# Optimization experiments

Measured on AMD Instinct MI355X. Metric: run time of the kernel, lower is better.

## Reference

```python
import jax, jax.numpy as jnp
import numpy as np

N_HEADS = 8  # head_dim = 640 / 8 = 80


def _split_heads(x):
    # [B, S, D] -> [B, H, S, D/H]
    B, S, D = x.shape
    return x.reshape(B, S, N_HEADS, D // N_HEADS).transpose(0, 2, 1, 3)


def _merge_heads(x):
    # [B, H, S, d] -> [B, S, H*d]
    B, H, S, d = x.shape
    return x.transpose(0, 2, 1, 3).reshape(B, S, H * d)


def setup_inputs() -> dict:
    key = jax.random.key(0)
    ks = jax.random.split(key, 12)
    B, S, D, C, A = 4, 2048, 640, 768, 16

    def w(k, fan_in, fan_out, s=1.0):
        return (jax.random.normal(k, (fan_in, fan_out), jnp.float32) / np.sqrt(fan_in) * s)

    return {
        "hidden_states": jax.random.normal(ks[0], (B, S, D), jnp.float32),
        "au_embedding": jax.random.normal(ks[1], (B, A, C), jnp.float32),
        "w_q": w(ks[2], D, D),
        "w_k": w(ks[3], D, D),
        "w_v": w(ks[4], D, D),
        "w_ak": w(ks[5], C, D),
        "w_av": w(ks[6], C, D),
        "w_g1": w(ks[7], D, D // 2),
        "b_g1": jnp.zeros((D // 2,), jnp.float32),
        "w_g2": w(ks[8], D // 2, D, s=0.02),  # near-zero per nn.init.zeros_
        "b_g2": jnp.full((D,), -1.5, jnp.float32),  # per nn.init.constant_(-1.5)
        "w_out": w(ks[9], D, D),
        "b_out": jnp.zeros((D,), jnp.float32),
        "temperature": jnp.full((1,), 5.0, jnp.float32),
    }


def reference(hidden_states, au_embedding, w_q, w_k, w_v, w_ak, w_av,
              w_g1, b_g1, w_g2, b_g2, w_out, b_out, temperature):
    au_scale = 1.0
    residual = hidden_states

    q = _split_heads(hidden_states @ w_q)  # [B,H,S,d]
    k = _split_heads(hidden_states @ w_k)
    v = _split_heads(hidden_states @ w_v)
    d = q.shape[-1]
    scale = 1.0 / jnp.sqrt(jnp.asarray(d, q.dtype))  # attn.scale = head_dim**-0.5

    # main self-attention: QK^T * scale -> softmax -> PV
    probs = jax.nn.softmax(jnp.einsum('bhqd,bhkd->bhqk', q, k) * scale, axis=-1)
    hs = _merge_heads(jnp.einsum('bhqk,bhkd->bhqd', probs, v))  # [B,S,D]

    # AU cross-attention with temperature-scaled logits
    au_k = _split_heads(au_embedding @ w_ak)  # [B,H,A,d]
    au_v = _split_heads(au_embedding @ w_av)
    scaled_alpha = scale * temperature[0]
    au_probs = jax.nn.softmax(jnp.einsum('bhqd,bhkd->bhqk', q, au_k) * scaled_alpha, axis=-1)
    au_hs = _merge_heads(jnp.einsum('bhqk,bhkd->bhqd', au_probs, au_v))  # [B,S,D]

    # gated MLP fusion: sigmoid(Linear(SiLU(Linear(au_hs))))
    gate = jax.nn.sigmoid(jax.nn.silu(au_hs @ w_g1 + b_g1) @ w_g2 + b_g2)
    hs = hs + au_scale * (gate * au_hs)

    hs = hs @ w_out + b_out  # to_out[0]; to_out[1] dropout is identity in eval
    return hs + residual  # residual_connection=True, rescale_output_factor=1.0
```

## Files before the change

### kernel.cpp

```cpp
#include <hip/hip_runtime.h>
#include <stdint.h>

typedef __attribute__((ext_vector_type(8))) short short8;
typedef __attribute__((ext_vector_type(4))) short short4v;
typedef __attribute__((ext_vector_type(4))) float f32x4;
typedef __attribute__((ext_vector_type(2))) uint32_t u32x2;

#define DEV static __device__ __forceinline__

DEV short f2bf(float f) {
  union { float f; uint32_t u; } v; v.f = f;
  uint32_t r = (v.u + 0x7fffu + ((v.u >> 16) & 1u)) >> 16;
  return (short)(uint16_t)r;
}
DEV float bf2f(short s) {
  union { uint32_t u; float f; } v; v.u = ((uint32_t)(uint16_t)s) << 16;
  return v.f;
}
DEV uint32_t fbits(float f) { union { float f; uint32_t u; } v; v.f = f; return v.u; }
DEV int imin(int a, int b) { return a < b ? a : b; }
DEV int xcd_swz(int bid, int nwg) {
  int q8 = nwg >> 3, r8 = nwg & 7;
  int xcd = bid & 7, lin = bid >> 3;
  return (xcd < r8 ? xcd * (q8 + 1) : r8 * (q8 + 1) + (xcd - r8) * q8) + lin;
}
DEV int detect_flag(const uint32_t* src, int t) {
  __shared__ int cnt;
  if (t == 0) cnt = 0;
  __syncthreads();
  uint32_t u = src[t & 255];
  int e = (int)((u >> 7) & 0xffu);
  if (e >= 110 && e <= 135) atomicAdd(&cnt, 1);
  __syncthreads();
  return cnt > 128;
}


struct WDesc { const void* src; short* dst; int K, N, dstride, tile0; };
struct WTable { WDesc d[8]; };

__global__ __launch_bounds__(256) void k_prep(
    const void* __restrict__ hidden, const void* __restrict__ auemb,
    short* __restrict__ HSB, short* __restrict__ AUB, WTable tb,
    const void* b1, const void* b2, const void* b3, const void* tp,
    float* B1, float* B2, float* B3, float* T) {
  const int t = threadIdx.x;
  const int isbf = detect_flag((const uint32_t*)hidden, t);
  const int bid = blockIdx.x;

  if (bid < 5168) {
    int i = bid * 256 + t;
    const void* src; short* dst;
    if (i < 1310720) { src = hidden; dst = HSB; }
    else { src = auemb; dst = AUB; i -= 1310720; }
    if (isbf) {
      ((short4v*)dst)[i] = ((const short4v*)src)[i];
    } else {
      f32x4 v = ((const f32x4*)src)[i];
      short4v o;
      o[0] = f2bf(v[0]); o[1] = f2bf(v[1]); o[2] = f2bf(v[2]); o[3] = f2bf(v[3]);
      ((short4v*)dst)[i] = o;
    }
  } else if (bid < 8128) {
    __shared__ float tile[32][33];
    int tid = bid - 5168;
    int idx = 0;
#pragma unroll
    for (int i = 1; i < 8; i++) if (tid >= tb.d[i].tile0) idx = i;
    WDesc wd = tb.d[idx];
    int local = tid - wd.tile0;
    int ntiles = wd.N >> 5;
    int n0 = (local % ntiles) * 32, k0 = (local / ntiles) * 32;
    int tx = t & 31, ty = t >> 5;
#pragma unroll
    for (int i = 0; i < 4; i++) {
      int r = k0 + ty + i * 8, c = n0 + tx;
      float v = 0.f;
      if (r < wd.K && c < wd.N)
        v = isbf ? bf2f(((const short*)wd.src)[(size_t)r * wd.N + c])
                 : ((const float*)wd.src)[(size_t)r * wd.N + c];
      tile[ty + i * 8][tx] = v;
    }
    __syncthreads();
#pragma unroll
    for (int i = 0; i < 4; i++) {
      int n = n0 + ty + i * 8, k = k0 + tx;
      if (n < wd.N && k < wd.K) wd.dst[(size_t)n * wd.dstride + k] = f2bf(tile[tx][ty + i * 8]);
    }
  } else {
    int i = (bid - 8128) * 256 + t;
    const void* s; float* d; int j;
    if (i < 320) { s = b1; d = B1; j = i; }
    else if (i < 960) { s = b2; d = B2; j = i - 320; }
    else if (i < 1600) { s = b3; d = B3; j = i - 960; }
    else if (i == 1600) { s = tp; d = T; j = 0; }
    else return;
    d[j] = isbf ? bf2f(((const short*)s)[j]) : ((const float*)s)[j];
  }
}

template <int EPI>
DEV void gemm_core(const short* __restrict__ A, const short* __restrict__ Wt,
                   void* __restrict__ Cout, int M, int N, int K, int m0, int n0,
                   const float* __restrict__ bias, const short* __restrict__ x1,
                   const short* __restrict__ x2, const short* __restrict__ res) {
  __shared__ __align__(16) short As[128 * 64];
  __shared__ __align__(16) short Bs[128 * 64];
  const int t = threadIdx.x;
  const int w = t >> 6, ln = t & 63;
  const int wm = w >> 1, wn = w & 1;
  const int lrow = ln & 15, lg = ln >> 4;

  f32x4 acc[4][4];
#pragma unroll
  for (int i = 0; i < 4; i++)
#pragma unroll
    for (int j = 0; j < 4; j++) acc[i][j] = (f32x4){0.f, 0.f, 0.f, 0.f};

  for (int k0 = 0; k0 < K; k0 += 64) {
    __syncthreads();
#pragma unroll
    for (int c = 0; c < 4; c++) {
      int cc = c * 256 + t;
      int r = cc >> 3, col = (cc & 7) * 8;
      int ra = imin(m0 + r, M - 1);
      int rb = imin(n0 + r, N - 1);
      __builtin_amdgcn_global_load_lds(
          (const __attribute__((address_space(1))) void*)(A + (size_t)ra * K + k0 + col),
          (__attribute__((address_space(3))) void*)&As[(c * 256 + w * 64) * 8],
          16, 0, 0);
      __builtin_amdgcn_global_load_lds(
          (const __attribute__((address_space(1))) void*)(Wt + (size_t)rb * K + k0 + col),
          (__attribute__((address_space(3))) void*)&Bs[(c * 256 + w * 64) * 8],
          16, 0, 0);
    }
    __syncthreads();
    short8 af[4][2], bfr[4][2];
#pragma unroll
    for (int i = 0; i < 4; i++)
#pragma unroll
      for (int kk = 0; kk < 2; kk++) {
        af[i][kk] = *(const short8*)&As[(wm * 64 + i * 16 + lrow) * 64 + lg * 8 + kk * 32];
        bfr[i][kk] = *(const short8*)&Bs[(wn * 64 + i * 16 + lrow) * 64 + lg * 8 + kk * 32];
      }
    __builtin_amdgcn_s_setprio(1);
#pragma unroll
    for (int kk = 0; kk < 2; kk++)
#pragma unroll
      for (int i = 0; i < 4; i++)
#pragma unroll
        for (int j = 0; j < 4; j++)
          acc[i][j] = __builtin_amdgcn_mfma_f32_16x16x32_bf16(af[i][kk], bfr[j][kk], acc[i][j], 0, 0, 0);
    __builtin_amdgcn_s_setprio(0);
  }

  const int rb0 = m0 + wm * 64 + lg * 4;
#pragma unroll
  for (int i = 0; i < 4; i++) {
#pragma unroll
    for (int j = 0; j < 4; j++) {
      int col = n0 + wn * 64 + j * 16 + lrow;
      if (col >= N) continue;
#pragma unroll
      for (int r = 0; r < 4; r++) {
        int row = rb0 + i * 16 + r;
        if (row >= M) continue;
        float v = acc[i][j][r];
        size_t off = (size_t)row * N + col;
        if (EPI == 0) {
          ((short*)Cout)[off] = f2bf(v);
        } else if (EPI == 1) {
          float x = v + bias[col];
          ((short*)Cout)[off] = f2bf(x / (1.f + __expf(-x)));
        } else if (EPI == 2) {
          float g = 1.f / (1.f + __expf(-(v + bias[col])));
          ((short*)Cout)[off] = f2bf(bf2f(x1[off]) + g * bf2f(x2[off]));
        } else {
          ((float*)Cout)[off] = v + bias[col] + bf2f(res[off]);
        }
      }
    }
  }
}

template <int EPI>
__global__ __launch_bounds__(256) void k_gemm_bt(
    const short* __restrict__ A, const short* __restrict__ Wt, void* __restrict__ Cout,
    int M, int N, int K, int nbx,
    const float* __restrict__ bias, const short* __restrict__ x1,
    const short* __restrict__ x2, const short* __restrict__ res) {
  const int swz = xcd_swz(blockIdx.x, gridDim.x);
  gemm_core<EPI>(A, Wt, Cout, M, N, K, (swz / nbx) * 128, (swz % nbx) * 128,
                 bias, x1, x2, res);
}

__global__ __launch_bounds__(256) void k_gemm_fused(
    const short* __restrict__ A0, const short* __restrict__ W0, short* __restrict__ C0,
    const short* __restrict__ A1, const short* __restrict__ W1, short* __restrict__ C1) {
  const int bid = blockIdx.x;
  if (bid < 960) {
    int swz = xcd_swz(bid, 960);
    gemm_core<0>(A0, W0, C0, 8192, 1920, 640, (swz / 15) * 128, (swz % 15) * 128,
                 nullptr, nullptr, nullptr, nullptr);
  } else {
    int local = bid - 960;
    gemm_core<0>(A1, W1, C1, 64, 1280, 768, 0, local * 128,
                 nullptr, nullptr, nullptr, nullptr);
  }
}

__global__ __launch_bounds__(256) void k_vt_au(const short* __restrict__ qkv,
                                               short* __restrict__ vt,
                                               const short* __restrict__ aukv,
                                               const float* __restrict__ temp,
                                               short* __restrict__ auhs) {
  __shared__ __align__(16) short SH[20480];
  const int bid = blockIdx.x;
  const int t = threadIdx.x;

  if (bid < 512) {
    short* T = SH;
    const int st = bid & 15, bh = bid >> 4;
    const int b = bh >> 3, h = bh & 7;
    for (int c = t; c < 1280; c += 256) {
      int r = c / 10, blk = c % 10;
      *(short8*)&T[r * 80 + blk * 8] =
          *(const short8*)(qkv + (size_t)(b * 2048 + st * 128 + r) * 1920 + 1280 + h * 80 + blk * 8);
    }
    __syncthreads();
    for (int c = t; c < 1280; c += 256) {
      int dd = c % 80, qc = (c / 80) * 8;
      short8 v;
#pragma unroll
      for (int i = 0; i < 8; i++) {
        int q = qc + i;
        int tile = q >> 6, p = q & 63;
        int src = (tile << 6) + (p >> 2) + ((p & 3) << 4);
        v[i] = T[src * 80 + dd];
      }
      *(short8*)(vt + ((size_t)bh * 80 + dd) * 2048 + st * 128 + qc) = v;
    }
  } else {
    short* aK = SH;
    short* aV = SH + 16 * 640;
    const int bid2 = bid - 512;
    const int sx = bid2 & 63, b = bid2 >> 6;
    for (int c = t; c < 2560; c += 256) {
      int arr = c / 1280, cc = c - arr * 1280;
      int r = cc / 80, blk = cc % 80;
      const short* s = aukv + (size_t)(b * 16 + r) * 1280 + arr * 640 + blk * 8;
      short* d = (arr ? aV : aK) + r * 640 + blk * 8;
      *(short8*)d = *(const short8*)s;
    }
    __syncthreads();
    const int sl = t & 31, h = t >> 5;
    const int s = sx * 32 + sl;
    const float alpha = 0.111803398875f * temp[0];
    const float LOG2E = 1.4426950408889634f;

    float qf[80];
    {
      const short* q = qkv + (size_t)(b * 2048 + s) * 1920 + h * 80;
#pragma unroll
      for (int c = 0; c < 10; c++) {
        short8 v = *(const short8*)(q + c * 8);
#pragma unroll
        for (int j = 0; j < 8; j++) qf[c * 8 + j] = bf2f(v[j]);
      }
    }
    float lgt[16];
#pragma unroll
    for (int a = 0; a < 16; a++) {
      const short* kr = &aK[a * 640 + h * 80];
      float acc = 0.f;
#pragma unroll
      for (int c = 0; c < 10; c++) {
        short8 v = *(const short8*)(kr + c * 8);
#pragma unroll
        for (int j = 0; j < 8; j++) acc += qf[c * 8 + j] * bf2f(v[j]);
      }
      lgt[a] = acc * alpha;
    }
    float m = lgt[0];
#pragma unroll
    for (int a = 1; a < 16; a++) m = fmaxf(m, lgt[a]);
    float se = 0.f;
#pragma unroll
    for (int a = 0; a < 16; a++) { lgt[a] = exp2f((lgt[a] - m) * LOG2E); se += lgt[a]; }
    float inv = 1.f / se;

    float o[80];
#pragma unroll
    for (int i = 0; i < 80; i++) o[i] = 0.f;
#pragma unroll
    for (int a = 0; a < 16; a++) {
      float pa = lgt[a] * inv;
      const short* vr = &aV[a * 640 + h * 80];
#pragma unroll
      for (int c = 0; c < 10; c++) {
        short8 v = *(const short8*)(vr + c * 8);
#pragma unroll
        for (int j = 0; j < 8; j++) o[c * 8 + j] += pa * bf2f(v[j]);
      }
    }
    short* op = auhs + (size_t)(b * 2048 + s) * 640 + h * 80;
#pragma unroll
    for (int c = 0; c < 10; c++) {
      short8 v;
#pragma unroll
      for (int j = 0; j < 8; j++) v[j] = f2bf(o[c * 8 + j]);
      *(short8*)(op + c * 8) = v;
    }
  }
}

__global__ __launch_bounds__(512) void k_attn(const short* __restrict__ qkv,
                                              const short* __restrict__ vt,
                                              short* __restrict__ outp) {
  __shared__ __align__(16) short Ks[64 * 104];
  __shared__ __align__(16) char Vs[80 * 128];
  __shared__ __align__(16) char Ps[8][2048];

  const int swzb = xcd_swz(blockIdx.x, 512);
  const int qt = swzb & 15, bh = swzb >> 4;
  const int b = bh >> 3, h = bh & 7;
  const int t = threadIdx.x, w = t >> 6, ln = t & 63;
  const int lg = ln >> 4, lr = ln & 15;
  const float sc2 = 0.111803398875f * 1.4426950408889634f;
  const float SHIFT2 = 32.0f;

  short8 qfrag[3];
  {
    const short* qrow = qkv + (size_t)(b * 2048 + qt * 128 + w * 16 + lr) * 1920 + h * 80;
#pragma unroll
    for (int ks = 0; ks < 3; ks++) {
      int off = ks * 32 + lg * 8;
      short8 v = {0, 0, 0, 0, 0, 0, 0, 0};
      if (off < 80) v = *(const short8*)(qrow + off);
      qfrag[ks] = v;
    }
  }

  const short* kbase = qkv + (size_t)b * 2048 * 1920 + 640 + h * 80;
  const short* vbase = vt + (size_t)bh * 80 * 2048;

  int kr0 = t / 12, kb0 = t % 12;
  int kr1 = (t + 512) / 12, kb1 = (t + 512) % 12;
  int vr0 = t >> 3, vb0 = t & 7;
  int vr1 = (t + 512) >> 3, vb1 = (t + 512) & 7;
  const bool kv1 = (t < 256), vv1 = (t < 128);

  short8 kreg0 = {0,0,0,0,0,0,0,0}, kreg1 = kreg0, vreg0 = kreg0, vreg1 = kreg0;

  if (kb0 < 10) kreg0 = *(const short8*)(kbase + (size_t)kr0 * 1920 + kb0 * 8);
  if (kv1 && kb1 < 10) kreg1 = *(const short8*)(kbase + (size_t)kr1 * 1920 + kb1 * 8);
  vreg0 = *(const short8*)(vbase + (size_t)vr0 * 2048 + vb0 * 8);
  if (vv1) vreg1 = *(const short8*)(vbase + (size_t)vr1 * 2048 + vb1 * 8);

  f32x4 oacc[5];
#pragma unroll
  for (int f = 0; f < 5; f++) oacc[f] = (f32x4){0.f, 0.f, 0.f, 0.f};
  float psacc[4] = {0.f, 0.f, 0.f, 0.f};

  for (int kt = 0; kt < 32; kt++) {
    __syncthreads();
    *(short8*)&Ks[kr0 * 104 + kb0 * 8] = kreg0;
    if (kv1) *(short8*)&Ks[kr1 * 104 + kb1 * 8] = kreg1;
    {
      int dst0 = (vr0 * 128 + vb0 * 16) ^ ((vr0 & 7) << 4);
      *(short8*)&Vs[dst0] = vreg0;
      if (vv1) {
        int dst1 = (vr1 * 128 + vb1 * 16) ^ ((vr1 & 7) << 4);
        *(short8*)&Vs[dst1] = vreg1;
      }
    }
    __syncthreads();

    if (kt < 31) {
      const short* kb2 = kbase + (size_t)(kt + 1) * 64 * 1920;
      const short* vb2 = vbase + (size_t)(kt + 1) * 64;
      if (kb0 < 10) kreg0 = *(const short8*)(kb2 + (size_t)kr0 * 1920 + kb0 * 8);
      if (kv1 && kb1 < 10) kreg1 = *(const short8*)(kb2 + (size_t)kr1 * 1920 + kb1 * 8);
      vreg0 = *(const short8*)(vb2 + (size_t)vr0 * 2048 + vb0 * 8);
      if (vv1) vreg1 = *(const short8*)(vb2 + (size_t)vr1 * 2048 + vb1 * 8);
    }

    f32x4 sf[4];
#pragma unroll
    for (int j = 0; j < 4; j++) sf[j] = (f32x4){0.f, 0.f, 0.f, 0.f};
    __builtin_amdgcn_s_setprio(1);
#pragma unroll
    for (int ks = 0; ks < 3; ks++) {
#pragma unroll
      for (int j = 0; j < 4; j++) {
        short8 bk = *(const short8*)&Ks[(j * 16 + lr) * 104 + ks * 32 + lg * 8];
        sf[j] = __builtin_amdgcn_mfma_f32_16x16x32_bf16(qfrag[ks], bk, sf[j], 0, 0, 0);
      }
    }
    __builtin_amdgcn_s_setprio(0);

    char* Pw = Ps[w];
#pragma unroll
    for (int r = 0; r < 4; r++) {
      int row = lg * 4 + r;
      float p0 = exp2f(sf[0][r] * sc2 - SHIFT2);
      float p1 = exp2f(sf[1][r] * sc2 - SHIFT2);
      float p2 = exp2f(sf[2][r] * sc2 - SHIFT2);
      float p3 = exp2f(sf[3][r] * sc2 - SHIFT2);
      psacc[r] += (p0 + p1) + (p2 + p3);
      u32x2 pk;
      pk[0] = (fbits(p0) >> 16) | (fbits(p1) & 0xffff0000u);
      pk[1] = (fbits(p2) >> 16) | (fbits(p3) & 0xffff0000u);
      int addr = (row * 128 + lr * 8) ^ ((row & 7) << 4);
      *(u32x2*)&Pw[addr] = pk;
    }

    __builtin_amdgcn_s_setprio(1);
#pragma unroll
    for (int ks = 0; ks < 2; ks++) {
      short8 ap = *(const short8*)&Pw[(lr * 128 + ks * 64 + lg * 16) ^ ((lr & 7) << 4)];
#pragma unroll
      for (int f = 0; f < 5; f++) {
        int vrow = f * 16 + lr;
        short8 bv = *(const short8*)&Vs[(vrow * 128 + ks * 64 + lg * 16) ^ ((vrow & 7) << 4)];
        oacc[f] = __builtin_amdgcn_mfma_f32_16x16x32_bf16(ap, bv, oacc[f], 0, 0, 0);
      }
    }
    __builtin_amdgcn_s_setprio(0);
  }

  float lrowv[4];
#pragma unroll
  for (int r = 0; r < 4; r++) {
    float sum = psacc[r];
#pragma unroll
    for (int off = 8; off >= 1; off >>= 1) sum += __shfl_xor(sum, off, 64);
    lrowv[r] = sum;
  }

#pragma unroll
  for (int f = 0; f < 5; f++) {
#pragma unroll
    for (int r = 0; r < 4; r++) {
      int q = qt * 128 + w * 16 + lg * 4 + r;
      float o = oacc[f][r] / lrowv[r];
      outp[(size_t)(b * 2048 + q) * 640 + h * 80 + f * 16 + lr] = f2bf(o);
    }
  }
}

extern "C" void kernel_launch(void* const* d_in, const int* in_sizes, int n_in,
                              void* d_out, int out_size, void* d_ws, size_t ws_size,
                              hipStream_t stream) {
  (void)in_sizes; (void)n_in; (void)out_size; (void)ws_size;

  const void* hidden = d_in[0];
  const void* auemb  = d_in[1];

  char* ws = (char*)d_ws;
  float* BG1  = (float*)(ws + 1024);
  float* BG2  = (float*)(ws + 4096);
  float* BOUT = (float*)(ws + 8192);
  float* TEMP = (float*)(ws + 12288);

  size_t o = 16384;
  short* HSB = (short*)(ws + o);    o += 10485760;
  short* AUB = (short*)(ws + o);    o += 98304;
  short* WQKVT = (short*)(ws + o);  o += 2457600;
  short* WAKVT = (short*)(ws + o);  o += 1966080;
  short* WG1T = (short*)(ws + o);   o += 409600;
  short* WG2T = (short*)(ws + o);   o += 409600;
  short* WOUTT = (short*)(ws + o);  o += 819200;
  short* QKV = (short*)(ws + o);    o += 31457280;
  short* VT = (short*)(ws + o);     o += 10485760;
  short* AUKV = (short*)(ws + o);   o += 163840;
  short* HSATTN = (short*)(ws + o); o += 10485760;
  short* AUHS = (short*)(ws + o);   o += 10485760;
  short* G1 = QKV;
  short* HSMIX = QKV + 5242880;

  WTable tb;
  tb.d[0] = { d_in[2],  WQKVT,              640, 640, 640, 0    };
  tb.d[1] = { d_in[3],  WQKVT + 409600,     640, 640, 640, 400  };
  tb.d[2] = { d_in[4],  WQKVT + 819200,     640, 640, 640, 800  };
  tb.d[3] = { d_in[5],  WAKVT,              768, 640, 768, 1200 };
  tb.d[4] = { d_in[6],  WAKVT + 640 * 768,  768, 640, 768, 1680 };
  tb.d[5] = { d_in[7],  WG1T,               640, 320, 640, 2160 };
  tb.d[6] = { d_in[9],  WG2T,               320, 640, 320, 2360 };
  tb.d[7] = { d_in[11], WOUTT,              640, 640, 640, 2560 };

  k_prep<<<8135, 256, 0, stream>>>(hidden, auemb, HSB, AUB, tb,
                                   d_in[8], d_in[10], d_in[12], d_in[13],
                                   BG1, BG2, BOUT, TEMP);
  k_gemm_fused<<<970, 256, 0, stream>>>(HSB, WQKVT, QKV, AUB, WAKVT, AUKV);
  k_vt_au<<<768, 256, 0, stream>>>(QKV, VT, AUKV, TEMP, AUHS);
  k_attn<<<512, 512, 0, stream>>>(QKV, VT, HSATTN);
  k_gemm_bt<1><<<192, 256, 0, stream>>>(AUHS, WG1T, G1, 8192, 320, 640, 3,
                                        BG1, nullptr, nullptr, nullptr);
  k_gemm_bt<2><<<320, 256, 0, stream>>>(G1, WG2T, HSMIX, 8192, 640, 320, 5,
                                        BG2, HSATTN, AUHS, nullptr);
  k_gemm_bt<3><<<320, 256, 0, stream>>>(HSMIX, WOUTT, d_out, 8192, 640, 640, 5,
                                        BOUT, nullptr, nullptr, HSB);
}
```

Baseline: 308.5 us.

## Fuse gate GEMM1 into attention launch and double-buffer attention K/V tiles

Merges the first gate-MLP GEMM into the attention kernel as 192 extra blocks, so it runs alongside attention in one launch and fills idle CUs. The K/V shared tiles in attention become double-buffered, which removes one barrier per key tile. gemm_core now takes shared buffers as arguments and masks the upper 256 threads when it runs in a 512-thread block. G1 moves to its own workspace region so it no longer aliases QKV, which attention is still reading. In exchange, the GEMM blocks leave half their threads idle and the kernel uses 64KB of shared memory, which may lower occupancy.

```diff
diff --git a/kernel.cpp b/kernel.cpp
--- a/kernel.cpp
+++ b/kernel.cpp
@@ -100,14 +100,14 @@
 }
 
 template <int EPI>
-DEV void gemm_core(const short* __restrict__ A, const short* __restrict__ Wt,
+DEV void gemm_core(short* __restrict__ As, short* __restrict__ Bs,
+                   const short* __restrict__ A, const short* __restrict__ Wt,
                    void* __restrict__ Cout, int M, int N, int K, int m0, int n0,
                    const float* __restrict__ bias, const short* __restrict__ x1,
                    const short* __restrict__ x2, const short* __restrict__ res) {
-  __shared__ __align__(16) short As[128 * 64];
-  __shared__ __align__(16) short Bs[128 * 64];
   const int t = threadIdx.x;
-  const int w = t >> 6, ln = t & 63;
+  const bool act = t < 256;
+  const int w = (t >> 6) & 3, ln = t & 63;
   const int wm = w >> 1, wn = w & 1;
   const int lrow = ln & 15, lg = ln >> 4;
 
@@ -119,41 +119,46 @@
 
   for (int k0 = 0; k0 < K; k0 += 64) {
     __syncthreads();
-#pragma unroll
-    for (int c = 0; c < 4; c++) {
-      int cc = c * 256 + t;
-      int r = cc >> 3, col = (cc & 7) * 8;
-      int ra = imin(m0 + r, M - 1);
-      int rb = imin(n0 + r, N - 1);
-      __builtin_amdgcn_global_load_lds(
-          (const __attribute__((address_space(1))) void*)(A + (size_t)ra * K + k0 + col),
-          (__attribute__((address_space(3))) void*)&As[(c * 256 + w * 64) * 8],
-          16, 0, 0);
-      __builtin_amdgcn_global_load_lds(
-          (const __attribute__((address_space(1))) void*)(Wt + (size_t)rb * K + k0 + col),
-          (__attribute__((address_space(3))) void*)&Bs[(c * 256 + w * 64) * 8],
-          16, 0, 0);
+    if (act) {
+#pragma unroll
+      for (int c = 0; c < 4; c++) {
+        int cc = c * 256 + t;
+        int r = cc >> 3, col = (cc & 7) * 8;
+        int ra = imin(m0 + r, M - 1);
+        int rb = imin(n0 + r, N - 1);
+        __builtin_amdgcn_global_load_lds(
+            (const __attribute__((address_space(1))) void*)(A + (size_t)ra * K + k0 + col),
+            (__attribute__((address_space(3))) void*)&As[(c * 256 + w * 64) * 8],
+            16, 0, 0);
+        __builtin_amdgcn_global_load_lds(
+            (const __attribute__((address_space(1))) void*)(Wt + (size_t)rb * K + k0 + col),
+            (__attribute__((address_space(3))) void*)&Bs[(c * 256 + w * 64) * 8],
+            16, 0, 0);
+      }
     }
     __syncthreads();
-    short8 af[4][2], bfr[4][2];
-#pragma unroll
-    for (int i = 0; i < 4; i++)
-#pragma unroll
-      for (int kk = 0; kk < 2; kk++) {
-        af[i][kk] = *(const short8*)&As[(wm * 64 + i * 16 + lrow) * 64 + lg * 8 + kk * 32];
-        bfr[i][kk] = *(const short8*)&Bs[(wn * 64 + i * 16 + lrow) * 64 + lg * 8 + kk * 32];
-      }
-    __builtin_amdgcn_s_setprio(1);
-#pragma unroll
-    for (int kk = 0; kk < 2; kk++)
+    if (act) {
+      short8 af[4][2], bfr[4][2];
 #pragma unroll
       for (int i = 0; i < 4; i++)
 #pragma unroll
-        for (int j = 0; j < 4; j++)
-          acc[i][j] = __builtin_amdgcn_mfma_f32_16x16x32_bf16(af[i][kk], bfr[j][kk], acc[i][j], 0, 0, 0);
-    __builtin_amdgcn_s_setprio(0);
-  }
-
+        for (int kk = 0; kk < 2; kk++) {
+          af[i][kk] = *(const short8*)&As[(wm * 64 + i * 16 + lrow) * 64 + lg * 8 + kk * 32];
+          bfr[i][kk] = *(const short8*)&Bs[(wn * 64 + i * 16 + lrow) * 64 + lg * 8 + kk * 32];
+        }
+      __builtin_amdgcn_s_setprio(1);
+#pragma unroll
+      for (int kk = 0; kk < 2; kk++)
+#pragma unroll
+        for (int i = 0; i < 4; i++)
+#pragma unroll
+          for (int j = 0; j < 4; j++)
+            acc[i][j] = __builtin_amdgcn_mfma_f32_16x16x32_bf16(af[i][kk], bfr[j][kk], acc[i][j], 0, 0, 0);
+      __builtin_amdgcn_s_setprio(0);
+    }
+  }
+
+  if (!act) return;
   const int rb0 = m0 + wm * 64 + lg * 4;
 #pragma unroll
   for (int i = 0; i < 4; i++) {
@@ -189,22 +194,26 @@
     int M, int N, int K, int nbx,
     const float* __restrict__ bias, const short* __restrict__ x1,
     const short* __restrict__ x2, const short* __restrict__ res) {
+  __shared__ __align__(16) short As[128 * 64];
+  __shared__ __align__(16) short Bs[128 * 64];
   const int swz = xcd_swz(blockIdx.x, gridDim.x);
-  gemm_core<EPI>(A, Wt, Cout, M, N, K, (swz / nbx) * 128, (swz % nbx) * 128,
+  gemm_core<EPI>(As, Bs, A, Wt, Cout, M, N, K, (swz / nbx) * 128, (swz % nbx) * 128,
                  bias, x1, x2, res);
 }
 
 __global__ __launch_bounds__(256) void k_gemm_fused(
     const short* __restrict__ A0, const short* __restrict__ W0, short* __restrict__ C0,
     const short* __restrict__ A1, const short* __restrict__ W1, short* __restrict__ C1) {
+  __shared__ __align__(16) short As[128 * 64];
+  __shared__ __align__(16) short Bs[128 * 64];
   const int bid = blockIdx.x;
   if (bid < 960) {
     int swz = xcd_swz(bid, 960);
-    gemm_core<0>(A0, W0, C0, 8192, 1920, 640, (swz / 15) * 128, (swz % 15) * 128,
+    gemm_core<0>(As, Bs, A0, W0, C0, 8192, 1920, 640, (swz / 15) * 128, (swz % 15) * 128,
                  nullptr, nullptr, nullptr, nullptr);
   } else {
     int local = bid - 960;
-    gemm_core<0>(A1, W1, C1, 64, 1280, 768, 0, local * 128,
+    gemm_core<0>(As, Bs, A1, W1, C1, 64, 1280, 768, 0, local * 128,
                  nullptr, nullptr, nullptr, nullptr);
   }
 }
@@ -314,12 +323,26 @@
   }
 }
 
-__global__ __launch_bounds__(512) void k_attn(const short* __restrict__ qkv,
-                                              const short* __restrict__ vt,
-                                              short* __restrict__ outp) {
-  __shared__ __align__(16) short Ks[64 * 104];
-  __shared__ __align__(16) char Vs[80 * 128];
-  __shared__ __align__(16) char Ps[8][2048];
+__global__ __launch_bounds__(512) void k_attn_g1(
+    const short* __restrict__ qkv, const short* __restrict__ vt,
+    short* __restrict__ outp,
+    const short* __restrict__ auhs, const short* __restrict__ wg1t,
+    short* __restrict__ g1, const float* __restrict__ bg1) {
+  __shared__ __align__(16) char SH[65536];
+
+  if (blockIdx.x >= 512) {
+    int local = (int)blockIdx.x - 512;
+    gemm_core<1>((short*)SH, (short*)(SH + 32768), auhs, wg1t, g1,
+                 8192, 320, 640, (local / 3) * 128, (local % 3) * 128,
+                 bg1, nullptr, nullptr, nullptr);
+    return;
+  }
+
+  short* KsB0 = (short*)SH;
+  short* KsB1 = (short*)(SH + 13312);
+  char* VsB0 = SH + 26624;
+  char* VsB1 = SH + 36864;
+  char* PsB = SH + 47104;
 
   const int swzb = xcd_swz(blockIdx.x, 512);
   const int qt = swzb & 15, bh = swzb >> 4;
@@ -363,7 +386,8 @@
   float psacc[4] = {0.f, 0.f, 0.f, 0.f};
 
   for (int kt = 0; kt < 32; kt++) {
-    __syncthreads();
+    short* Ks = (kt & 1) ? KsB1 : KsB0;
+    char* Vs = (kt & 1) ? VsB1 : VsB0;
     *(short8*)&Ks[kr0 * 104 + kb0 * 8] = kreg0;
     if (kv1) *(short8*)&Ks[kr1 * 104 + kb1 * 8] = kreg1;
     {
@@ -399,7 +423,7 @@
     }
     __builtin_amdgcn_s_setprio(0);
 
-    char* Pw = Ps[w];
+    char* Pw = PsB + w * 2048;
 #pragma unroll
     for (int r = 0; r < 4; r++) {
       int row = lg * 4 + r;
@@ -476,8 +500,8 @@
   short* AUKV = (short*)(ws + o);   o += 163840;
   short* HSATTN = (short*)(ws + o); o += 10485760;
   short* AUHS = (short*)(ws + o);   o += 10485760;
-  short* G1 = QKV;
-  short* HSMIX = QKV + 5242880;
+  short* G1 = (short*)(ws + o);     o += 5242880;
+  short* HSMIX = QKV;
 
   WTable tb;
   tb.d[0] = { d_in[2],  WQKVT,              640, 640, 640, 0    };
@@ -494,9 +518,7 @@
                                    BG1, BG2, BOUT, TEMP);
   k_gemm_fused<<<970, 256, 0, stream>>>(HSB, WQKVT, QKV, AUB, WAKVT, AUKV);
   k_vt_au<<<768, 256, 0, stream>>>(QKV, VT, AUKV, TEMP, AUHS);
-  k_attn<<<512, 512, 0, stream>>>(QKV, VT, HSATTN);
-  k_gemm_bt<1><<<192, 256, 0, stream>>>(AUHS, WG1T, G1, 8192, 320, 640, 3,
-                                        BG1, nullptr, nullptr, nullptr);
+  k_attn_g1<<<704, 512, 0, stream>>>(QKV, VT, HSATTN, AUHS, WG1T, G1, BG1);
   k_gemm_bt<2><<<320, 256, 0, stream>>>(G1, WG2T, HSMIX, 8192, 640, 320, 5,
                                         BG2, HSATTN, AUHS, nullptr);
   k_gemm_bt<3><<<320, 256, 0, stream>>>(HSMIX, WOUTT, d_out, 8192, 640, 640, 5,
```

Result: slower. 336.2 us (+9.0%).
